# Kernel tuning notes

Measured on AMD Instinct MI355X. Metric: run time of the kernel, lower is better.

## Reference

```python
import jax, jax.numpy as jnp
import numpy as np

N_HEADS = 8
OUT_FEATURES = 64
LEAKY_SLOPE = 0.2
MASK_FILL = -1e9


def setup_inputs() -> dict:
    key = jax.random.key(0)
    k_h, k_adj, k_W, k_a = jax.random.split(key, 4)
    B, N, F_IN = 1, 4096, 128
    h = jax.random.normal(k_h, (B, N, F_IN), dtype=jnp.float32)
    adj_mat = jax.random.randint(k_adj, (N, N), 0, 2, dtype=jnp.int32)
    # glorot-style scaled params
    W = jax.random.normal(k_W, (F_IN, OUT_FEATURES * N_HEADS), dtype=jnp.float32) * (1.0 / np.sqrt(F_IN))
    a = jax.random.normal(k_a, (N_HEADS, 2 * OUT_FEATURES, 1), dtype=jnp.float32) * (1.0 / np.sqrt(2 * OUT_FEATURES))
    return {"h": h, "adj_mat": adj_mat, "W": W, "a": a}


def reference(h, adj_mat, W, a):
    B, N, _ = h.shape
    heads = a.shape[0]
    out = a.shape[1] // 2
    # linear transform + head split (same reshape order as tf.reshape)
    ht = jnp.reshape(h @ W, (-1, heads, N, out))            # (B, heads, N, out)
    # additive attention scores
    src = jnp.einsum('bhnf,hfo->bhno', ht, a[:, :out, :])    # (B, heads, N, 1)
    tgt = jnp.einsum('bhnf,hfo->bhno', ht, a[:, out:, :])    # (B, heads, N, 1)
    e = src + jnp.swapaxes(tgt, -1, -2)                      # (B, heads, N, N)
    e = jnp.where(e > 0, e, LEAKY_SLOPE * e)                 # leaky_relu
    e = jnp.where(adj_mat > 0, e, MASK_FILL)                 # adjacency mask
    attention = jax.nn.softmax(e, axis=-1)
    h_prime = attention @ ht                                 # (B, heads, N, out)
    return h_prime
```

## Files before the change

kernel.cpp:

```cpp
#include <hip/hip_runtime.h>
#include <stdint.h>

#define HT_STRIDE 262144
#define LOG2E 1.4426950408889634f

typedef __attribute__((ext_vector_type(8))) short bf16x8;
typedef __attribute__((ext_vector_type(4))) float f32x4;
typedef __attribute__((ext_vector_type(2))) float f32x2;

__device__ __forceinline__ unsigned short f2bf(float f) {
    unsigned int u = __float_as_uint(f);
    u += 0x7FFFu + ((u >> 16) & 1u);
    return (unsigned short)(u >> 16);
}

__device__ __forceinline__ float exp2_fast(float e) {
#if __has_builtin(__builtin_amdgcn_exp2f)
    return __builtin_amdgcn_exp2f(e);
#else
    return __expf(e * 0.6931471805599453f);
#endif
}

__global__ void __launch_bounds__(256) k_fused(const float* __restrict__ h,
                                               const int* __restrict__ adj,
                                               const float* __restrict__ W,
                                               const float* __restrict__ aW,
                                               float* __restrict__ ess,
                                               float* __restrict__ ets,
                                               unsigned short* __restrict__ htT2,
                                               unsigned int* __restrict__ abm) {
    __shared__ unsigned int ldsT[1024];
    __shared__ float hs[8][128];
    __shared__ float ldsA[64][66];
    __shared__ float redS[4][64];
    __shared__ float redT[4][64];
    const int t = threadIdx.x;

    if ((blockIdx.x & 1) == 0) {
        const int eid = (int)blockIdx.x >> 1;
        const int lane = t & 63;
        const int w = t >> 6;
        const int sb = eid >> 3;
        const int cq = eid & 7;
        for (int rr = 0; rr < 16; ++rr) {
            const int* arow = adj + (sb * 64 + w * 16 + rr) * 4096 + cq * 512;
            int v[8];
            #pragma unroll
            for (int j = 0; j < 8; ++j) v[j] = arow[j * 64 + lane];
            #pragma unroll
            for (int j = 0; j < 8; ++j) {
                unsigned long long m = __ballot(v[j] > 0);
                if (lane < 2)
                    ldsT[(2 * j + lane) * 64 + rr * 4 + w] = (unsigned int)(m >> (lane * 32));
            }
        }
        __syncthreads();
        ((uint4*)(abm + (sb * 128 + cq * 16) * 64))[t] = ((uint4*)ldsT)[t];
    } else {
        const int bid2 = (int)blockIdx.x >> 1;
        const int n0 = bid2 * 8;
        const int p0 = bid2 * 64;
        const int hd = p0 >> 12;
        const int m0 = p0 & 4095;

        {
            float4 v = ((const float4*)(h + n0 * 128))[t];
            int e = t * 4;
            int r = e >> 7, f = e & 127;
            hs[r][f + 0] = v.x; hs[r][f + 1] = v.y;
            hs[r][f + 2] = v.z; hs[r][f + 3] = v.w;
        }
        __syncthreads();

        float acc0[8], acc1[8];
        #pragma unroll
        for (int r = 0; r < 8; ++r) { acc0[r] = 0.f; acc1[r] = 0.f; }
        const float2* Wf = (const float2*)W;
        float2 wpb[4];
        #pragma unroll
        for (int j = 0; j < 4; ++j) wpb[j] = Wf[j * 256 + t];
        for (int fb = 0; fb < 32; ++fb) {
            const int fn = ((fb + 1) & 31) * 4;
            float2 wn[4];
            #pragma unroll
            for (int j = 0; j < 4; ++j) wn[j] = Wf[(fn + j) * 256 + t];
            #pragma unroll
            for (int j = 0; j < 4; ++j) {
                const int f = fb * 4 + j;
                #pragma unroll
                for (int r = 0; r < 8; ++r) {
                    float hv = hs[r][f];
                    acc0[r] = fmaf(hv, wpb[j].x, acc0[r]);
                    acc1[r] = fmaf(hv, wpb[j].y, acc1[r]);
                }
            }
            #pragma unroll
            for (int j = 0; j < 4; ++j) wpb[j] = wn[j];
        }
        {
            const int ns = t >> 5;
            const int o = (2 * t) & 63;
            #pragma unroll
            for (int r = 0; r < 8; ++r) {
                *(float2*)&ldsA[r * 8 + ns][o] = make_float2(acc0[r], acc1[r]);
            }
        }
        __syncthreads();

        {
            const int r = t & 63, og = t >> 6;
            float sdot = 0.f, gdot = 0.f;
            #pragma unroll
            for (int k = 0; k < 16; ++k) {
                int o = og * 16 + k;
                float hv = ldsA[r][o];
                sdot = fmaf(hv, aW[hd * 128 + o], sdot);
                gdot = fmaf(hv, aW[hd * 128 + 64 + o], gdot);
            }
            redS[og][r] = sdot; redT[og][r] = gdot;
        }
        __syncthreads();
        if (t < 64) {
            float sp = (redS[0][t] + redS[1][t] + redS[2][t] + redS[3][t]) * LOG2E;
            ess[hd * 8192 + m0 + t]        = exp2_fast(sp);
            ess[hd * 8192 + 4096 + m0 + t] = exp2_fast(0.2f * sp);
        } else if (t < 128) {
            int r = t - 64;
            float tv = (redT[0][r] + redT[1][r] + redT[2][r] + redT[3][r]) * LOG2E;
            ets[hd * 8192 + m0 + r]        = exp2_fast(tv);
            ets[hd * 8192 + 4096 + m0 + r] = exp2_fast(0.2f * tv);
        }

        unsigned short* d = htT2 + (hd * 128 + (m0 >> 5)) * 2048;
        #pragma unroll
        for (int i = 0; i < 16; ++i) {
            int id = t + 256 * i;
            int mi = id & 31, o = (id >> 5) & 63, ct = id >> 11;
            d[ct * 2048 + o * 32 + mi] = f2bf(ldsA[mi + 32 * ct][o]);
        }
    }
}

__global__ void __launch_bounds__(512) k_attn(const unsigned int* __restrict__ abm,
                                              const unsigned short* __restrict__ htT2,
                                              const float* __restrict__ ess,
                                              const float* __restrict__ ets,
                                              float* __restrict__ out) {
    __shared__ __align__(16) float smem[8192];

    const int t = threadIdx.x;
    const int wv = t >> 6;
    const int rh = wv >> 2;
    const int kq = wv & 3;
    const int lane = t & 63;
    const int li = lane & 15;
    const int quad = lane >> 4;
    const int head = blockIdx.x & 7;
    const int s32 = blockIdx.x >> 3;
    const int s64 = s32 >> 1, half = s32 & 1;
    const int i0 = s32 * 32;

    {
        const float4* esrc = (const float4*)(ets + head * 8192);
        float4* edst = (float4*)smem;
        #pragma unroll
        for (int i = 0; i < 4; ++i) edst[t + 512 * i] = esrc[t + 512 * i];
    }

    const float e1 = ess[head * 8192 + i0 + 16 * rh + li];
    const float e2 = ess[head * 8192 + 4096 + i0 + 16 * rh + li];
    const f32x2 esv  = (f32x2){e1, e1};
    const f32x2 es2v = (f32x2){e2, e2};

    f32x4 acc[4];
    #pragma unroll
    for (int i = 0; i < 4; ++i) acc[i] = (f32x4){0.f, 0.f, 0.f, 0.f};
    f32x4 apd = (f32x4){0.f, 0.f, 0.f, 0.f};

    const uint4 onesw = {0x3F803F80u, 0x3F803F80u, 0x3F803F80u, 0x3F803F80u};
    const bf16x8 aones = __builtin_bit_cast(bf16x8, onesw);

    const uint4* ap = (const uint4*)(htT2 + head * HT_STRIDE) + (li * 4 + quad);
    const unsigned int* bmp = abm + s64 * 8192 + li * 4 + half * 2 + rh;

    __syncthreads();

    const int c0 = kq * 32;
    #pragma unroll 1
    for (int ci = 0; ci < 32; ++ci) {
        const int c = c0 + ci;
        uint4 av0 = ap[c * 256 + 0];
        uint4 av1 = ap[c * 256 + 64];
        uint4 av2 = ap[c * 256 + 128];
        uint4 av3 = ap[c * 256 + 192];
        const unsigned int bw = bmp[c * 64];

        const float4* etp  = (const float4*)(smem + c * 32 + quad * 8);
        const float4* et2p = (const float4*)(smem + 4096 + c * 32 + quad * 8);
        float4 ta = etp[0],  tb = etp[1];
        float4 ua = et2p[0], ub = et2p[1];
        const f32x2 etq[4]  = {(f32x2){ta.x, ta.y}, (f32x2){ta.z, ta.w},
                               (f32x2){tb.x, tb.y}, (f32x2){tb.z, tb.w}};
        const f32x2 et2q[4] = {(f32x2){ua.x, ua.y}, (f32x2){ua.z, ua.w},
                               (f32x2){ub.x, ub.y}, (f32x2){ub.z, ub.w}};

        const unsigned int wq = bw >> (quad * 8);
        unsigned int pk[4];
        #pragma unroll
        for (int m = 0; m < 4; ++m) {
            f32x2 p1 = etq[m] * esv;
            f32x2 p2 = et2q[m] * es2v;
            float w0 = fmaxf(p1[0], p2[0]);
            float w1 = fmaxf(p1[1], p2[1]);
            unsigned int pkm;
            asm("v_cvt_pk_bf16_f32 %0, %1, %2" : "=v"(pkm) : "v"(w0), "v"(w1));
            const int j0 = 2 * m, j1 = 2 * m + 1;
            const unsigned int lo = (unsigned int)((int)(wq << (31 - j0)) >> 31);
            const unsigned int hi = (unsigned int)((int)(wq << (31 - j1)) >> 31);
            pk[m] = pkm & ((lo & 0x0000FFFFu) | (hi & 0xFFFF0000u));
        }
        uint4 bv; bv.x = pk[0]; bv.y = pk[1]; bv.z = pk[2]; bv.w = pk[3];
        bf16x8 bfrag = __builtin_bit_cast(bf16x8, bv);
        apd    = __builtin_amdgcn_mfma_f32_16x16x32_bf16(aones, bfrag, apd, 0, 0, 0);
        acc[0] = __builtin_amdgcn_mfma_f32_16x16x32_bf16(__builtin_bit_cast(bf16x8, av0), bfrag, acc[0], 0, 0, 0);
        acc[1] = __builtin_amdgcn_mfma_f32_16x16x32_bf16(__builtin_bit_cast(bf16x8, av1), bfrag, acc[1], 0, 0, 0);
        acc[2] = __builtin_amdgcn_mfma_f32_16x16x32_bf16(__builtin_bit_cast(bf16x8, av2), bfrag, acc[2], 0, 0, 0);
        acc[3] = __builtin_amdgcn_mfma_f32_16x16x32_bf16(__builtin_bit_cast(bf16x8, av3), bfrag, acc[3], 0, 0, 0);
    }

    __syncthreads();
    if (kq != 0) {
        float* cb = smem + ((rh * 3 + (kq - 1)) * 64 + lane) * 20;
        #pragma unroll
        for (int i = 0; i < 4; ++i) ((f32x4*)cb)[i] = acc[i];
        cb[16] = apd[0];
    }
    __syncthreads();
    if (kq == 0) {
        float pd = apd[0];
        #pragma unroll
        for (int q = 0; q < 3; ++q) {
            const float* cb = smem + ((rh * 3 + q) * 64 + lane) * 20;
            #pragma unroll
            for (int i = 0; i < 4; ++i) acc[i] += ((const f32x4*)cb)[i];
            pd += cb[16];
        }
        const float rd = 1.0f / pd;
        float4* op = (float4*)(out + head * HT_STRIDE + (i0 + 16 * rh + li) * 64);
        #pragma unroll
        for (int f = 0; f < 4; ++f) {
            f32x4 a = acc[f];
            op[f * 4 + quad] = make_float4(a[0] * rd, a[1] * rd, a[2] * rd, a[3] * rd);
        }
    }
}

extern "C" void kernel_launch(void* const* d_in, const int* in_sizes, int n_in,
                              void* d_out, int out_size, void* d_ws, size_t ws_size,
                              hipStream_t stream) {
    const float* h   = (const float*)d_in[0];
    const int*   adj = (const int*)d_in[1];
    const float* W   = (const float*)d_in[2];
    const float* aW  = (const float*)d_in[3];
    float* out = (float*)d_out;

    char* ws = (char*)d_ws;
    float* ess = (float*)(ws);
    float* ets = (float*)(ws + 262144);
    unsigned int*   abm  = (unsigned int*)(ws + 524288);
    unsigned short* htT2 = (unsigned short*)(ws + 2621440);

    hipLaunchKernelGGL(k_fused, dim3(1024), dim3(256), 0, stream,
                       h, adj, W, aW, ess, ets, htT2, abm);
    hipLaunchKernelGGL(k_attn,  dim3(1024), dim3(512), 0, stream,
                       abm, htT2, ess, ets, out);
}
```

Measured before the change: 184.9 us.

## Stage ht tiles in LDS with double buffering and widen rows per block

```diff
diff --git a/kernel.cpp b/kernel.cpp
--- a/kernel.cpp
+++ b/kernel.cpp
@@ -147,19 +147,18 @@
                                               const float* __restrict__ ess,
                                               const float* __restrict__ ets,
                                               float* __restrict__ out) {
-    __shared__ __align__(16) float smem[8192];
+    __shared__ __align__(16) float smem[12288];
 
     const int t = threadIdx.x;
     const int wv = t >> 6;
-    const int rh = wv >> 2;
-    const int kq = wv & 3;
+    const int kh = wv >> 2;
+    const int g  = wv & 3;
     const int lane = t & 63;
     const int li = lane & 15;
     const int quad = lane >> 4;
     const int head = blockIdx.x & 7;
-    const int s32 = blockIdx.x >> 3;
-    const int s64 = s32 >> 1, half = s32 & 1;
-    const int i0 = s32 * 32;
+    const int s64 = blockIdx.x >> 3;
+    const int i0 = s64 * 64;
 
     {
         const float4* esrc = (const float4*)(ets + head * 8192);
@@ -168,8 +167,8 @@
         for (int i = 0; i < 4; ++i) edst[t + 512 * i] = esrc[t + 512 * i];
     }
 
-    const float e1 = ess[head * 8192 + i0 + 16 * rh + li];
-    const float e2 = ess[head * 8192 + 4096 + i0 + 16 * rh + li];
+    const float e1 = ess[head * 8192 + i0 + 16 * g + li];
+    const float e2 = ess[head * 8192 + 4096 + i0 + 16 * g + li];
     const f32x2 esv  = (f32x2){e1, e1};
     const f32x2 es2v = (f32x2){e2, e2};
 
@@ -181,20 +180,31 @@
     const uint4 onesw = {0x3F803F80u, 0x3F803F80u, 0x3F803F80u, 0x3F803F80u};
     const bf16x8 aones = __builtin_bit_cast(bf16x8, onesw);
 
-    const uint4* ap = (const uint4*)(htT2 + head * HT_STRIDE) + (li * 4 + quad);
-    const unsigned int* bmp = abm + s64 * 8192 + li * 4 + half * 2 + rh;
+    const int sc  = t & 255;
+    const int skh = t >> 8;
+    const uint4* gtile = (const uint4*)(htT2 + head * HT_STRIDE);
+    float* bufb = smem + 8192;
+
+    uint4 stg0 = gtile[(skh * 64 + 0) * 256 + sc];
+    uint4 stgN = gtile[(skh * 64 + 1) * 256 + sc];
+    ((uint4*)(bufb + (skh * 2 + 0) * 1024))[sc] = stg0;
+
+    const unsigned int* bmp = abm + s64 * 8192 + g;
 
     __syncthreads();
 
-    const int c0 = kq * 32;
     #pragma unroll 1
-    for (int ci = 0; ci < 32; ++ci) {
-        const int c = c0 + ci;
-        uint4 av0 = ap[c * 256 + 0];
-        uint4 av1 = ap[c * 256 + 64];
-        uint4 av2 = ap[c * 256 + 128];
-        uint4 av3 = ap[c * 256 + 192];
-        const unsigned int bw = bmp[c * 64];
+    for (int ci = 0; ci < 64; ++ci) {
+        const int c = kh * 64 + ci;
+        const int cp = (ci < 62) ? (ci + 2) : 63;
+        uint4 stgF = gtile[(skh * 64 + cp) * 256 + sc];
+
+        const uint4* abuf = (const uint4*)(bufb + (kh * 2 + (ci & 1)) * 1024);
+        uint4 av0 = abuf[  0 + li * 4 + quad];
+        uint4 av1 = abuf[ 64 + li * 4 + quad];
+        uint4 av2 = abuf[128 + li * 4 + quad];
+        uint4 av3 = abuf[192 + li * 4 + quad];
+        const unsigned int bw = bmp[c * 64 + li * 4];
 
         const float4* etp  = (const float4*)(smem + c * 32 + quad * 8);
         const float4* et2p = (const float4*)(smem + 4096 + c * 32 + quad * 8);
@@ -227,27 +237,26 @@
         acc[1] = __builtin_amdgcn_mfma_f32_16x16x32_bf16(__builtin_bit_cast(bf16x8, av1), bfrag, acc[1], 0, 0, 0);
         acc[2] = __builtin_amdgcn_mfma_f32_16x16x32_bf16(__builtin_bit_cast(bf16x8, av2), bfrag, acc[2], 0, 0, 0);
         acc[3] = __builtin_amdgcn_mfma_f32_16x16x32_bf16(__builtin_bit_cast(bf16x8, av3), bfrag, acc[3], 0, 0, 0);
-    }
-
-    __syncthreads();
-    if (kq != 0) {
-        float* cb = smem + ((rh * 3 + (kq - 1)) * 64 + lane) * 20;
+
+        ((uint4*)(bufb + (skh * 2 + ((ci + 1) & 1)) * 1024))[sc] = stgN;
+        __syncthreads();
+        stgN = stgF;
+    }
+
+    if (kh == 1) {
+        float* cb = smem + (g * 64 + lane) * 20;
         #pragma unroll
         for (int i = 0; i < 4; ++i) ((f32x4*)cb)[i] = acc[i];
         cb[16] = apd[0];
     }
     __syncthreads();
-    if (kq == 0) {
-        float pd = apd[0];
-        #pragma unroll
-        for (int q = 0; q < 3; ++q) {
-            const float* cb = smem + ((rh * 3 + q) * 64 + lane) * 20;
-            #pragma unroll
-            for (int i = 0; i < 4; ++i) acc[i] += ((const f32x4*)cb)[i];
-            pd += cb[16];
-        }
+    if (kh == 0) {
+        const float* cb = smem + (g * 64 + lane) * 20;
+        #pragma unroll
+        for (int i = 0; i < 4; ++i) acc[i] += ((const f32x4*)cb)[i];
+        const float pd = apd[0] + cb[16];
         const float rd = 1.0f / pd;
-        float4* op = (float4*)(out + head * HT_STRIDE + (i0 + 16 * rh + li) * 64);
+        float4* op = (float4*)(out + head * HT_STRIDE + (i0 + 16 * g + li) * 64);
         #pragma unroll
         for (int f = 0; f < 4; ++f) {
             f32x4 a = acc[f];
@@ -273,6 +282,6 @@
 
     hipLaunchKernelGGL(k_fused, dim3(1024), dim3(256), 0, stream,
                        h, adj, W, aW, ess, ets, htT2, abm);
-    hipLaunchKernelGGL(k_attn,  dim3(1024), dim3(512), 0, stream,
+    hipLaunchKernelGGL(k_attn,  dim3(512),  dim3(512), 0, stream,
                        abm, htT2, ess, ets, out);
 }
```

Result: faster. 151.1 us (-18.3%).
